# Performance work log

Measured on AMD Instinct MI355X. Metric: run time of the kernel, lower is better.

## Reference

```python
import jax, jax.numpy as jnp
import numpy as np

D_MODEL = 1024
N_HEADS = 16
N_KV_HEADS = 4
HEAD_DIM = 64   # d_model // total_n_heads
KEY_DIM = 64    # defaults to head_dim
N_REP = N_HEADS // N_KV_HEADS
ATTN_SCALE = 1.0 / np.sqrt(HEAD_DIM)
B, S = 2, 2048


def apply_rope(x, cos, sin):
    # x: [B,S,H,Dh]; cos/sin: [S,Dh//2]; pairs are (x[2j], x[2j+1]) per llama-style apply_rotary_emb
    xr, xi = x[..., ::2], x[..., 1::2]
    c = cos[None, :, None, :]
    s = sin[None, :, None, :]
    out_r = xr * c - xi * s
    out_i = xr * s + xi * c
    return jnp.stack([out_r, out_i], axis=-1).reshape(x.shape)


def setup_inputs() -> dict:
    key = jax.random.key(0)
    ks = jax.random.split(key, 7)
    query = jax.random.normal(ks[0], (B, S, D_MODEL), jnp.float32)
    k_in = jax.random.normal(ks[1], (B, S, D_MODEL), jnp.float32)
    v_in = jax.random.normal(ks[2], (B, S, D_MODEL), jnp.float32)
    # real RoPE frequency tables (theta=10000)
    inv_freq = 1.0 / (10000.0 ** (np.arange(0, KEY_DIM, 2, dtype=np.float32) / KEY_DIM))
    ang = np.outer(np.arange(S, dtype=np.float32), inv_freq)  # [S, KEY_DIM//2]
    freqs_cos = jnp.asarray(np.cos(ang), jnp.float32)
    freqs_sin = jnp.asarray(np.sin(ang), jnp.float32)
    sc = D_MODEL ** -0.5
    wq = jax.random.normal(ks[3], (N_HEADS * KEY_DIM, D_MODEL), jnp.float32) * sc
    wk = jax.random.normal(ks[4], (N_KV_HEADS * KEY_DIM, D_MODEL), jnp.float32) * sc
    wv = jax.random.normal(ks[5], (N_KV_HEADS * HEAD_DIM, D_MODEL), jnp.float32) * sc
    wo = jax.random.normal(ks[6], (N_HEADS * HEAD_DIM, N_HEADS * HEAD_DIM), jnp.float32) * sc
    return {"query": query, "key": k_in, "value": v_in,
            "freqs_cos": freqs_cos, "freqs_sin": freqs_sin,
            "wq": wq, "wk": wk, "wv": wv, "wo": wo}


def reference(query, key, value, freqs_cos, freqs_sin, wq, wk, wv, wo):
    b, sq, _ = query.shape
    sk = key.shape[1]
    xq = (query @ wq.T).reshape(b, sq, N_HEADS, KEY_DIM)
    xk = (key @ wk.T).reshape(b, sk, N_KV_HEADS, KEY_DIM)
    xv = (value @ wv.T).reshape(b, sk, N_KV_HEADS, HEAD_DIM)
    xq = apply_rope(xq, freqs_cos, freqs_sin)
    xk = apply_rope(xk, freqs_cos, freqs_sin)
    # GQA: repeat kv heads (equivalent to torch repeat_kv expand+reshape)
    xk = jnp.repeat(xk, N_REP, axis=2)
    xv = jnp.repeat(xv, N_REP, axis=2)
    scores = jnp.einsum('bqhd,bkhd->bhqk', xq, xk) * ATTN_SCALE
    causal = jnp.tril(jnp.ones((sq, sk), dtype=bool))
    scores = jnp.where(causal[None, None, :, :], scores, -jnp.inf)
    attn = jax.nn.softmax(scores, axis=-1)
    out = jnp.einsum('bhqk,bkhd->bqhd', attn, xv).reshape(b, sq, N_HEADS * HEAD_DIM)
    return out @ wo.T
```

## Files before the change

### kernel.cpp

```cpp
#include <hip/hip_runtime.h>

#define DM 1024
#define NHEADS 16
#define NKVH 4
#define HDIM 64
#define NB 2
#define SEQ 2048
#define MTOK (NB*SEQ)

typedef __attribute__((ext_vector_type(4))) float f32x4;
typedef __attribute__((ext_vector_type(8))) short short8;
typedef unsigned short u16;
typedef unsigned int u32;

__device__ __forceinline__ u16 f2b(float f) {
  u32 i; __builtin_memcpy(&i, &f, 4);
  u32 r = i + 0x7fffu + ((i >> 16) & 1u);
  return (u16)(r >> 16);
}
__device__ __forceinline__ u32 cvtpk(float a, float b) {
  u32 r; asm("v_cvt_pk_bf16_f32 %0, %1, %2" : "=v"(r) : "v"(a), "v"(b)); return r;
}
__device__ __forceinline__ void gload16(const void* g, void* l) {
  __builtin_amdgcn_global_load_lds((const __attribute__((address_space(1))) u32*)g,
                                   (__attribute__((address_space(3))) u32*)l, 16, 0, 0);
}

__global__ __launch_bounds__(256) void gemm_qkv(const float* __restrict__ Aq, const float* __restrict__ Ak,
                                                const float* __restrict__ Av, const float* __restrict__ wq,
                                                const float* __restrict__ wk, const float* __restrict__ wv,
                                                const float* __restrict__ cosb, const float* __restrict__ sinb,
                                                u16* __restrict__ Qr, u16* __restrict__ Kr,
                                                u16* __restrict__ Vt) {
  __shared__ __attribute__((aligned(16))) u16 SH[13824];
  u16* As = SH;
  u16* Bs = SH + 4608;
  const int tid = threadIdx.x, lane = tid & 63, w = tid >> 6;
  const int wr = w >> 1, wc = w & 1, lo = lane & 15, hi = lane >> 4;
  const int bx = blockIdx.x, by = blockIdx.y;
  const int m0 = bx * 64;

  const float *Ap, *Wp;
  int n0, mode;
  if (by < 8) { Ap = Aq; Wp = wq; n0 = by * 128; mode = 0; }
  else if (by < 10) { Ap = Ak; Wp = wk; n0 = (by - 8) * 128; mode = 1; }
  else { Ap = Av; Wp = wv; n0 = (by - 10) * 128; mode = 2; }

  const int srw = tid >> 2, sc0 = (tid & 3) * 4;
  const float* Abase = Ap + (size_t)(m0 + srw) * DM + sc0;
  const float* Wbase = Wp + (size_t)(n0 + srw) * DM + sc0;

  f32x4 acc[2][4];
#pragma unroll
  for (int i = 0; i < 2; i++)
#pragma unroll
    for (int j = 0; j < 4; j++) acc[i][j] = (f32x4){0.f, 0.f, 0.f, 0.f};

  float4 ra[4], rb[8];
#pragma unroll
  for (int j = 0; j < 4; j++) ra[j] = *(const float4*)(Abase + j * 16);
#pragma unroll
  for (int s = 0; s < 2; s++)
#pragma unroll
    for (int j = 0; j < 4; j++) rb[s * 4 + j] = *(const float4*)(Wbase + (size_t)s * 64 * DM + j * 16);

  for (int ks = 0; ks < 16; ks++) {
#pragma unroll
    for (int j = 0; j < 4; j++) {
      u32 w2[2] = {cvtpk(ra[j].x, ra[j].y), cvtpk(ra[j].z, ra[j].w)};
      *(uint2*)&As[srw * 72 + sc0 + j * 16] = *(uint2*)w2;
    }
#pragma unroll
    for (int s = 0; s < 2; s++)
#pragma unroll
      for (int j = 0; j < 4; j++) {
        u32 w2[2] = {cvtpk(rb[s * 4 + j].x, rb[s * 4 + j].y), cvtpk(rb[s * 4 + j].z, rb[s * 4 + j].w)};
        *(uint2*)&Bs[(s * 64 + srw) * 72 + sc0 + j * 16] = *(uint2*)w2;
      }
    __syncthreads();
    if (ks < 15) {
      const int k1 = (ks + 1) * 64;
#pragma unroll
      for (int j = 0; j < 4; j++) ra[j] = *(const float4*)(Abase + k1 + j * 16);
#pragma unroll
      for (int s = 0; s < 2; s++)
#pragma unroll
        for (int j = 0; j < 4; j++)
          rb[s * 4 + j] = *(const float4*)(Wbase + (size_t)s * 64 * DM + k1 + j * 16);
    }
    short8 af[2][2], bfr[4][2];
#pragma unroll
    for (int mi = 0; mi < 2; mi++)
#pragma unroll
      for (int kk = 0; kk < 2; kk++)
        af[mi][kk] = *(const short8*)(&As[(wr * 32 + mi * 16 + lo) * 72 + kk * 32 + hi * 8]);
#pragma unroll
    for (int ni = 0; ni < 4; ni++)
#pragma unroll
      for (int kk = 0; kk < 2; kk++)
        bfr[ni][kk] = *(const short8*)(&Bs[(wc * 64 + ni * 16 + lo) * 72 + kk * 32 + hi * 8]);
    __builtin_amdgcn_s_setprio(1);
#pragma unroll
    for (int mi = 0; mi < 2; mi++)
#pragma unroll
      for (int ni = 0; ni < 4; ni++) {
        acc[mi][ni] = __builtin_amdgcn_mfma_f32_16x16x32_bf16(af[mi][0], bfr[ni][0], acc[mi][ni], 0, 0, 0);
        acc[mi][ni] = __builtin_amdgcn_mfma_f32_16x16x32_bf16(af[mi][1], bfr[ni][1], acc[mi][ni], 0, 0, 0);
      }
    __builtin_amdgcn_s_setprio(0);
    __syncthreads();
  }

  if (mode < 2) {
    const float scale = (mode == 0) ? 0.18033688f : 1.0f;
    u16* outp = (mode == 0) ? Qr : Kr;
    const int OH = (mode == 0) ? NHEADS : NKVH;
    const float sgn = (lo & 1) ? 1.0f : -1.0f;
#pragma unroll
    for (int ni = 0; ni < 4; ni++) {
      const int col = n0 + wc * 64 + ni * 16 + lo;
      const int h = col >> 6, d = col & 63, j = d >> 1;
#pragma unroll
      for (int mi = 0; mi < 2; mi++)
#pragma unroll
        for (int r = 0; r < 4; r++) {
          int row = m0 + wr * 32 + mi * 16 + hi * 4 + r;
          int srow = row & (SEQ - 1), bb = row >> 11;
          float v = acc[mi][ni][r];
          float pv = __shfl_xor(v, 1, 64);
          float c = cosb[srow * 32 + j];
          float s = sinb[srow * 32 + j];
          outp[((size_t)(bb * OH + h) * SEQ + srow) * 64 + d] = f2b((v * c + pv * s * sgn) * scale);
        }
    }
  } else {
    u16* Tt = SH;
#pragma unroll
    for (int mi = 0; mi < 2; mi++)
#pragma unroll
      for (int ni = 0; ni < 4; ni++) {
        const int cl = wc * 64 + ni * 16 + lo;
#pragma unroll
        for (int r = 0; r < 4; r++) {
          int rl = wr * 32 + mi * 16 + hi * 4 + r;
          Tt[cl * 72 + rl] = f2b(acc[mi][ni][r]);
        }
      }
    __syncthreads();
    const int dl = tid >> 1;
    const int sh2 = (tid & 1) * 32;
    const int dg = n0 + dl;
    const int kh = dg >> 6, drow = dg & 63;
    const int bb = m0 >> 11, sbase = m0 & (SEQ - 1);
    u16* dst = Vt + ((size_t)(bb * NKVH + kh) * 64 + drow) * SEQ + sbase + sh2;
#pragma unroll
    for (int i = 0; i < 4; i++)
      *(uint4*)(dst + i * 8) = *(const uint4*)&Tt[dl * 72 + sh2 + i * 8];
  }
}

__device__ __forceinline__ void softmax_pv(f32x4 (&sc)[4], float& m, float& lsp, f32x4 (&o)[4],
                                           const short8* vb0, const short8* vb1, int hi) {
  float lm = sc[0][0];
#pragma unroll
  for (int f = 0; f < 4; f++)
#pragma unroll
    for (int r = 0; r < 4; r++) lm = fmaxf(lm, sc[f][r]);
  if (__any(lm - m > 8.f)) {
    float mx = fmaxf(m, lm);
    mx = fmaxf(mx, __shfl_xor(mx, 16, 64));
    mx = fmaxf(mx, __shfl_xor(mx, 32, 64));
    float corr = exp2f(m - mx);
    m = mx;
    lsp *= corr;
    float corrq[4];
#pragma unroll
    for (int r = 0; r < 4; r++) corrq[r] = __shfl(corr, hi * 4 + r, 64);
#pragma unroll
    for (int nf = 0; nf < 4; nf++)
#pragma unroll
      for (int r = 0; r < 4; r++) o[nf][r] *= corrq[r];
  }
  float pv2[4][4];
#pragma unroll
  for (int f = 0; f < 4; f++)
#pragma unroll
    for (int r = 0; r < 4; r++) {
      pv2[f][r] = exp2f(sc[f][r] - m);
      lsp += pv2[f][r];
    }
  union { u32 u[4]; short8 s8; } pa0, pa1;
#pragma unroll
  for (int t = 0; t < 4; t++) {
    int fsel = t >> 1, r0 = 2 * (t & 1);
    pa0.u[t] = cvtpk(pv2[fsel][r0], pv2[fsel][r0 + 1]);
    pa1.u[t] = cvtpk(pv2[2 + fsel][r0], pv2[2 + fsel][r0 + 1]);
  }
  __builtin_amdgcn_s_setprio(1);
#pragma unroll
  for (int nf = 0; nf < 4; nf++) {
    o[nf] = __builtin_amdgcn_mfma_f32_16x16x32_bf16(pa0.s8, vb0[nf], o[nf], 0, 0, 0);
    o[nf] = __builtin_amdgcn_mfma_f32_16x16x32_bf16(pa1.s8, vb1[nf], o[nf], 0, 0, 0);
  }
  __builtin_amdgcn_s_setprio(0);
}

__global__ __launch_bounds__(256, 2) void attn_kernel(const u16* __restrict__ Q, const u16* __restrict__ Kb,
                                                      const u16* __restrict__ Vt, u16* __restrict__ AO) {
  __shared__ __attribute__((aligned(16))) u16 Ks[2][4096];
  __shared__ __attribute__((aligned(16))) u16 Vs[2][4096];
  const int tid = threadIdx.x;
  const int w = tid >> 6, lane = tid & 63;
  const int lo = lane & 15, hi = lane >> 4;
  const int bh = blockIdx.x;
  const int b = bh >> 4, h = bh & 15, kh = h >> 2;
  const int p = blockIdx.y;
  const int tA = p, tB = 31 - p;
  const int q0A = tA * 64 + w * 16;
  const int q0B = tB * 64 + w * 16;
  const u16* Qp = Q + (size_t)bh * SEQ * 64;
  const u16* Kp = Kb + (size_t)(b * NKVH + kh) * SEQ * 64;
  const u16* Vp = Vt + (size_t)(b * NKVH + kh) * 64 * SEQ;

  short8 qfA[2], qfB[2];
#pragma unroll
  for (int kk = 0; kk < 2; kk++) {
    qfA[kk] = *(const short8*)(Qp + (size_t)(q0A + lo) * 64 + kk * 32 + hi * 8);
    qfB[kk] = *(const short8*)(Qp + (size_t)(q0B + lo) * 64 + kk * 32 + hi * 8);
  }

  f32x4 oA[4], oB[4];
#pragma unroll
  for (int nf = 0; nf < 4; nf++) { oA[nf] = (f32x4){0.f,0.f,0.f,0.f}; oB[nf] = (f32x4){0.f,0.f,0.f,0.f}; }
  float mA = -__builtin_inff(), lspA = 0.f;
  float mB = -__builtin_inff(), lspB = 0.f;

  auto key = [](int row) { return (row & 3) | (((row >> 3) & 1) << 2); };
  auto stage = [&](int kv0, int bufi) {
#pragma unroll
    for (int s = 0; s < 2; s++) {
      int base = s * 4096 + w * 1024;
      int o2 = base + (lane << 4);
      int row = o2 >> 7;
      int gg = ((o2 >> 4) & 7) ^ key(row);
      gload16(Kp + (size_t)(kv0 + row) * 64 + gg * 8, (char*)&Ks[bufi][0] + base);
      gload16(Vp + (size_t)row * SEQ + kv0 + gg * 8, (char*)&Vs[bufi][0] + base);
    }
  };
  auto lds8 = [&](const u16* S, int row, int col8) {
    return *(const short8*)(S + row * 64 + (col8 ^ (key(row) << 3)));
  };

  int krow[4];
#pragma unroll
  for (int f = 0; f < 4; f++)
    krow[f] = 32 * (f >> 1) + 8 * (lo >> 2) + 4 * (f & 1) + (lo & 3);

  const int nt = tB + 1;
  stage(0, 0);
  __syncthreads();

  for (int c = 0; c < nt; ++c) {
    const int cur = c & 1;
    const int kv0 = c * 64;
    if (c + 1 < nt) stage(kv0 + 64, cur ^ 1);

    short8 kf0[4], kf1[4];
#pragma unroll
    for (int f = 0; f < 4; f++) {
      kf0[f] = lds8(&Ks[cur][0], krow[f], hi * 8);
      kf1[f] = lds8(&Ks[cur][0], krow[f], 32 + hi * 8);
    }
    const bool actA = (c <= tA);

    f32x4 scB[4], scA[4];
#pragma unroll
    for (int f = 0; f < 4; f++) scB[f] = (f32x4){0.f,0.f,0.f,0.f};
    __builtin_amdgcn_s_setprio(1);
#pragma unroll
    for (int f = 0; f < 4; f++) {
      scB[f] = __builtin_amdgcn_mfma_f32_16x16x32_bf16(kf0[f], qfB[0], scB[f], 0, 0, 0);
      scB[f] = __builtin_amdgcn_mfma_f32_16x16x32_bf16(kf1[f], qfB[1], scB[f], 0, 0, 0);
    }
    __builtin_amdgcn_s_setprio(0);
    if (actA) {
#pragma unroll
      for (int f = 0; f < 4; f++) scA[f] = (f32x4){0.f,0.f,0.f,0.f};
      __builtin_amdgcn_s_setprio(1);
#pragma unroll
      for (int f = 0; f < 4; f++) {
        scA[f] = __builtin_amdgcn_mfma_f32_16x16x32_bf16(kf0[f], qfA[0], scA[f], 0, 0, 0);
        scA[f] = __builtin_amdgcn_mfma_f32_16x16x32_bf16(kf1[f], qfA[1], scA[f], 0, 0, 0);
      }
      __builtin_amdgcn_s_setprio(0);
    }

    short8 vb0[4], vb1[4];
#pragma unroll
    for (int nf = 0; nf < 4; nf++) {
      vb0[nf] = lds8(&Vs[cur][0], nf * 16 + lo, hi * 8);
      vb1[nf] = lds8(&Vs[cur][0], nf * 16 + lo, 32 + hi * 8);
    }

    if (c == tB) {
#pragma unroll
      for (int f = 0; f < 4; f++) {
        int kvb = kv0 + 32 * (f >> 1) + 8 * hi + 4 * (f & 1);
#pragma unroll
        for (int r = 0; r < 4; r++)
          if (kvb + r > q0B + lo) scB[f][r] = -__builtin_inff();
      }
    }
    softmax_pv(scB, mB, lspB, oB, vb0, vb1, hi);

    if (actA) {
      if (c == tA) {
#pragma unroll
        for (int f = 0; f < 4; f++) {
          int kvb = kv0 + 32 * (f >> 1) + 8 * hi + 4 * (f & 1);
#pragma unroll
          for (int r = 0; r < 4; r++)
            if (kvb + r > q0A + lo) scA[f][r] = -__builtin_inff();
        }
      }
      softmax_pv(scA, mA, lspA, oA, vb0, vb1, hi);
    }
    __syncthreads();
  }

#pragma unroll
  for (int t2 = 0; t2 < 2; t2++) {
    float lsp = t2 ? lspB : lspA;
    const int q0 = t2 ? q0B : q0A;
    f32x4* o = t2 ? oB : oA;
    lsp += __shfl_xor(lsp, 16, 64);
    lsp += __shfl_xor(lsp, 32, 64);
    float inv = 1.0f / lsp;
    float invq[4];
#pragma unroll
    for (int r = 0; r < 4; r++) invq[r] = __shfl(inv, hi * 4 + r, 64);
#pragma unroll
    for (int nf = 0; nf < 4; nf++)
#pragma unroll
      for (int r = 0; r < 4; r++) {
        int q = q0 + hi * 4 + r;
        int d = nf * 16 + lo;
        AO[((size_t)(b * SEQ + q) * NHEADS + h) * 64 + d] = f2b(o[nf][r] * invq[r]);
      }
  }
}

__global__ __launch_bounds__(256) void gemm_out(const u16* __restrict__ A, const float* __restrict__ W,
                                                float* __restrict__ Out) {
  __shared__ __attribute__((aligned(16))) u16 As[4096];
  __shared__ __attribute__((aligned(16))) u16 Bs[9216];
  const int tid = threadIdx.x, lane = tid & 63, w = tid >> 6;
  const int wr = w >> 1, wc = w & 1, lo = lane & 15, hi = lane >> 4;
  const int m0 = blockIdx.x * 64, n0 = blockIdx.y * 128;
  const int crow = lane >> 3;
  const int gsw = ((lane & 7) ^ crow) << 3;

  f32x4 acc[2][4];
#pragma unroll
  for (int i = 0; i < 2; i++)
#pragma unroll
    for (int j = 0; j < 4; j++) acc[i][j] = (f32x4){0.f, 0.f, 0.f, 0.f};

  const int srw = tid >> 2, sc0 = (tid & 3) * 4;
  const float* Wbase = W + (size_t)(n0 + srw) * DM + sc0;
  float4 rb[8];
#pragma unroll
  for (int s = 0; s < 2; s++)
#pragma unroll
    for (int j = 0; j < 4; j++) rb[s * 4 + j] = *(const float4*)(Wbase + (size_t)s * 64 * DM + j * 16);

  for (int ks = 0; ks < 16; ks++) {
    const int k0 = ks * 64;
#pragma unroll
    for (int cc = 0; cc < 2; ++cc) {
      int c = w * 2 + cc;
      gload16(A + (size_t)(m0 + c * 8 + crow) * DM + k0 + gsw, &As[c * 512]);
    }
#pragma unroll
    for (int s = 0; s < 2; s++)
#pragma unroll
      for (int j = 0; j < 4; j++) {
        u32 w2[2] = {cvtpk(rb[s * 4 + j].x, rb[s * 4 + j].y), cvtpk(rb[s * 4 + j].z, rb[s * 4 + j].w)};
        *(uint2*)&Bs[(s * 64 + srw) * 72 + sc0 + j * 16] = *(uint2*)w2;
      }
    __syncthreads();
    if (ks < 15) {
      const int k1 = k0 + 64;
#pragma unroll
      for (int s = 0; s < 2; s++)
#pragma unroll
        for (int j = 0; j < 4; j++)
          rb[s * 4 + j] = *(const float4*)(Wbase + (size_t)s * 64 * DM + k1 + j * 16);
    }
    short8 af[2][2], bfr[4][2];
#pragma unroll
    for (int mi = 0; mi < 2; mi++)
#pragma unroll
      for (int kk = 0; kk < 2; kk++)
        af[mi][kk] = *(const short8*)(&As[(wr * 32 + mi * 16 + lo) * 64 + (((kk * 4 + hi) ^ (lo & 7)) << 3)]);
#pragma unroll
    for (int ni = 0; ni < 4; ni++)
#pragma unroll
      for (int kk = 0; kk < 2; kk++)
        bfr[ni][kk] = *(const short8*)(&Bs[(wc * 64 + ni * 16 + lo) * 72 + kk * 32 + hi * 8]);
    __builtin_amdgcn_s_setprio(1);
#pragma unroll
    for (int mi = 0; mi < 2; mi++)
#pragma unroll
      for (int ni = 0; ni < 4; ni++) {
        acc[mi][ni] = __builtin_amdgcn_mfma_f32_16x16x32_bf16(af[mi][0], bfr[ni][0], acc[mi][ni], 0, 0, 0);
        acc[mi][ni] = __builtin_amdgcn_mfma_f32_16x16x32_bf16(af[mi][1], bfr[ni][1], acc[mi][ni], 0, 0, 0);
      }
    __builtin_amdgcn_s_setprio(0);
    __syncthreads();
  }

#pragma unroll
  for (int mi = 0; mi < 2; mi++)
#pragma unroll
    for (int ni = 0; ni < 4; ni++)
#pragma unroll
      for (int r = 0; r < 4; r++) {
        int row = m0 + wr * 32 + mi * 16 + hi * 4 + r;
        int col = n0 + wc * 64 + ni * 16 + lo;
        Out[(size_t)row * DM + col] = acc[mi][ni][r];
      }
}

extern "C" void kernel_launch(void* const* d_in, const int* in_sizes, int n_in,
                              void* d_out, int out_size, void* d_ws, size_t ws_size,
                              hipStream_t stream) {
  const float* query = (const float*)d_in[0];
  const float* key_ = (const float*)d_in[1];
  const float* value = (const float*)d_in[2];
  const float* fcos = (const float*)d_in[3];
  const float* fsin = (const float*)d_in[4];
  const float* wq = (const float*)d_in[5];
  const float* wk = (const float*)d_in[6];
  const float* wv = (const float*)d_in[7];
  const float* wo = (const float*)d_in[8];

  char* ws = (char*)d_ws;
  size_t off = 0;
  auto alloc = [&](size_t elems) {
    u16* p = (u16*)(ws + off);
    off = (off + elems * 2 + 255) & ~(size_t)255;
    return p;
  };
  u16* Qr = alloc((size_t)MTOK * DM);
  u16* Kr = alloc((size_t)NB * NKVH * SEQ * 64);
  u16* Vt = alloc((size_t)NB * NKVH * 64 * SEQ);
  u16* AO = alloc((size_t)MTOK * DM);

  gemm_qkv<<<dim3(64, 12), 256, 0, stream>>>(query, key_, value, wq, wk, wv,
                                             fcos, fsin, Qr, Kr, Vt);

  attn_kernel<<<dim3(NB * NHEADS, 16), 256, 0, stream>>>(Qr, Kr, Vt, AO);

  gemm_out<<<dim3(64, 8), 256, 0, stream>>>(AO, wo, (float*)d_out);
}
```

Before: 98.88 us.

## Pre-convert inputs and weights to bf16 and stage GEMM tiles via direct LDS loads

Adds a conversion kernel that turns the fp32 activations and all weights into bf16 buffers before the GEMMs. Both GEMMs then load tiles straight into swizzled LDS with global_load_lds instead of loading fp32 into registers and converting per tile, and their occupancy hints are raised. This removes per-tile conversion and register staging, at the cost of an extra kernel launch and a full extra read and write of the inputs. The attention kernel's blockIdx.y to tile-pair mapping is also reordered.

```diff
diff --git a/kernel.cpp b/kernel.cpp
--- a/kernel.cpp
+++ b/kernel.cpp
@@ -26,29 +26,76 @@
                                    (__attribute__((address_space(3))) u32*)l, 16, 0, 0);
 }
 
-__global__ __launch_bounds__(256) void gemm_qkv(const float* __restrict__ Aq, const float* __restrict__ Ak,
-                                                const float* __restrict__ Av, const float* __restrict__ wq,
-                                                const float* __restrict__ wk, const float* __restrict__ wv,
-                                                const float* __restrict__ cosb, const float* __restrict__ sinb,
-                                                u16* __restrict__ Qr, u16* __restrict__ Kr,
-                                                u16* __restrict__ Vt) {
-  __shared__ __attribute__((aligned(16))) u16 SH[13824];
+__device__ __forceinline__ void cvt8(const float* __restrict__ src, u16* __restrict__ dst, int i) {
+  float4 a = *(const float4*)(src + i);
+  float4 b = *(const float4*)(src + i + 4);
+  uint4 pk;
+  pk.x = cvtpk(a.x, a.y);
+  pk.y = cvtpk(a.z, a.w);
+  pk.z = cvtpk(b.x, b.y);
+  pk.w = cvtpk(b.z, b.w);
+  *(uint4*)(dst + i) = pk;
+}
+
+__global__ __launch_bounds__(256) void cvt_all(const float* __restrict__ q, const float* __restrict__ k,
+                                               const float* __restrict__ v, const float* __restrict__ wq,
+                                               const float* __restrict__ wk, const float* __restrict__ wv,
+                                               const float* __restrict__ wo, u16* oq, u16* ok, u16* ov,
+                                               u16* owq, u16* owk, u16* owv, u16* owo) {
+  const int ACT = (MTOK * DM) / 2048;
+  const int BIG = (DM * DM) / 2048;
+  const int SML = (256 * DM) / 2048;
+  int bid = blockIdx.x;
+  const float* s; u16* d;
+  if (bid < ACT) { s = q; d = oq; }
+  else if (bid < 2 * ACT) { s = k; d = ok; bid -= ACT; }
+  else if (bid < 3 * ACT) { s = v; d = ov; bid -= 2 * ACT; }
+  else {
+    bid -= 3 * ACT;
+    if (bid < BIG) { s = wq; d = owq; }
+    else if (bid < 2 * BIG) { s = wo; d = owo; bid -= BIG; }
+    else if (bid < 2 * BIG + SML) { s = wk; d = owk; bid -= 2 * BIG; }
+    else { s = wv; d = owv; bid -= 2 * BIG + SML; }
+  }
+  cvt8(s, d, (bid * 256 + threadIdx.x) * 8);
+}
+
+template<int NR>
+__device__ __forceinline__ void stage_tile(const u16* __restrict__ src, int k0, u16* lds,
+                                           int w, int lane) {
+#pragma unroll
+  for (int i = 0; i < NR / 32; i++) {
+    const int base = (i * 4 + w) * 1024;
+    const int row = (base >> 7) + (lane >> 3);
+    const int g = lane & 7;
+    gload16(src + (size_t)row * DM + k0 + ((g ^ (row & 7)) << 3), (char*)lds + base);
+  }
+}
+__device__ __forceinline__ short8 lds_frag(const u16* L, int row, int gr) {
+  return *(const short8*)(L + row * 64 + ((gr ^ (row & 7)) << 3));
+}
+
+__global__ __launch_bounds__(256, 3) void gemm_qkv(const u16* __restrict__ Aq, const u16* __restrict__ Ak,
+                                                   const u16* __restrict__ Av, const u16* __restrict__ wq,
+                                                   const u16* __restrict__ wk, const u16* __restrict__ wv,
+                                                   const float* __restrict__ cosb, const float* __restrict__ sinb,
+                                                   u16* __restrict__ Qr, u16* __restrict__ Kr,
+                                                   u16* __restrict__ Vt) {
+  __shared__ __attribute__((aligned(16))) u16 SH[12288];
   u16* As = SH;
-  u16* Bs = SH + 4608;
+  u16* Bs = SH + 4096;
   const int tid = threadIdx.x, lane = tid & 63, w = tid >> 6;
   const int wr = w >> 1, wc = w & 1, lo = lane & 15, hi = lane >> 4;
   const int bx = blockIdx.x, by = blockIdx.y;
   const int m0 = bx * 64;
 
-  const float *Ap, *Wp;
+  const u16 *Ap, *Wp;
   int n0, mode;
   if (by < 8) { Ap = Aq; Wp = wq; n0 = by * 128; mode = 0; }
   else if (by < 10) { Ap = Ak; Wp = wk; n0 = (by - 8) * 128; mode = 1; }
   else { Ap = Av; Wp = wv; n0 = (by - 10) * 128; mode = 2; }
-
-  const int srw = tid >> 2, sc0 = (tid & 3) * 4;
-  const float* Abase = Ap + (size_t)(m0 + srw) * DM + sc0;
-  const float* Wbase = Wp + (size_t)(n0 + srw) * DM + sc0;
+  const u16* Abase = Ap + (size_t)m0 * DM;
+  const u16* Wbase = Wp + (size_t)n0 * DM;
 
   f32x4 acc[2][4];
 #pragma unroll
@@ -56,49 +103,22 @@
 #pragma unroll
     for (int j = 0; j < 4; j++) acc[i][j] = (f32x4){0.f, 0.f, 0.f, 0.f};
 
-  float4 ra[4], rb[8];
-#pragma unroll
-  for (int j = 0; j < 4; j++) ra[j] = *(const float4*)(Abase + j * 16);
-#pragma unroll
-  for (int s = 0; s < 2; s++)
-#pragma unroll
-    for (int j = 0; j < 4; j++) rb[s * 4 + j] = *(const float4*)(Wbase + (size_t)s * 64 * DM + j * 16);
-
   for (int ks = 0; ks < 16; ks++) {
-#pragma unroll
-    for (int j = 0; j < 4; j++) {
-      u32 w2[2] = {cvtpk(ra[j].x, ra[j].y), cvtpk(ra[j].z, ra[j].w)};
-      *(uint2*)&As[srw * 72 + sc0 + j * 16] = *(uint2*)w2;
-    }
-#pragma unroll
-    for (int s = 0; s < 2; s++)
-#pragma unroll
-      for (int j = 0; j < 4; j++) {
-        u32 w2[2] = {cvtpk(rb[s * 4 + j].x, rb[s * 4 + j].y), cvtpk(rb[s * 4 + j].z, rb[s * 4 + j].w)};
-        *(uint2*)&Bs[(s * 64 + srw) * 72 + sc0 + j * 16] = *(uint2*)w2;
-      }
-    __syncthreads();
-    if (ks < 15) {
-      const int k1 = (ks + 1) * 64;
-#pragma unroll
-      for (int j = 0; j < 4; j++) ra[j] = *(const float4*)(Abase + k1 + j * 16);
-#pragma unroll
-      for (int s = 0; s < 2; s++)
-#pragma unroll
-        for (int j = 0; j < 4; j++)
-          rb[s * 4 + j] = *(const float4*)(Wbase + (size_t)s * 64 * DM + k1 + j * 16);
-    }
+    const int k0 = ks * 64;
+    stage_tile<64>(Abase, k0, As, w, lane);
+    stage_tile<128>(Wbase, k0, Bs, w, lane);
+    __syncthreads();
     short8 af[2][2], bfr[4][2];
 #pragma unroll
     for (int mi = 0; mi < 2; mi++)
 #pragma unroll
       for (int kk = 0; kk < 2; kk++)
-        af[mi][kk] = *(const short8*)(&As[(wr * 32 + mi * 16 + lo) * 72 + kk * 32 + hi * 8]);
+        af[mi][kk] = lds_frag(As, wr * 32 + mi * 16 + lo, kk * 4 + hi);
 #pragma unroll
     for (int ni = 0; ni < 4; ni++)
 #pragma unroll
       for (int kk = 0; kk < 2; kk++)
-        bfr[ni][kk] = *(const short8*)(&Bs[(wc * 64 + ni * 16 + lo) * 72 + kk * 32 + hi * 8]);
+        bfr[ni][kk] = lds_frag(Bs, wc * 64 + ni * 16 + lo, kk * 4 + hi);
     __builtin_amdgcn_s_setprio(1);
 #pragma unroll
     for (int mi = 0; mi < 2; mi++)
@@ -214,7 +234,8 @@
   const int lo = lane & 15, hi = lane >> 4;
   const int bh = blockIdx.x;
   const int b = bh >> 4, h = bh & 15, kh = h >> 2;
-  const int p = blockIdx.y;
+  const int yy = blockIdx.y;
+  const int p = (yy < 8) ? yy : 23 - yy;
   const int tA = p, tB = 31 - p;
   const int q0A = tA * 64 + w * 16;
   const int q0B = tB * 64 + w * 16;
@@ -350,64 +371,39 @@
   }
 }
 
-__global__ __launch_bounds__(256) void gemm_out(const u16* __restrict__ A, const float* __restrict__ W,
-                                                float* __restrict__ Out) {
-  __shared__ __attribute__((aligned(16))) u16 As[4096];
-  __shared__ __attribute__((aligned(16))) u16 Bs[9216];
+__global__ __launch_bounds__(256, 2) void gemm_out(const u16* __restrict__ A, const u16* __restrict__ W,
+                                                   float* __restrict__ Out) {
+  __shared__ __attribute__((aligned(16))) u16 SH[12288];
+  u16* As = SH;
+  u16* Bs = SH + 4096;
   const int tid = threadIdx.x, lane = tid & 63, w = tid >> 6;
   const int wr = w >> 1, wc = w & 1, lo = lane & 15, hi = lane >> 4;
   const int m0 = blockIdx.x * 64, n0 = blockIdx.y * 128;
-  const int crow = lane >> 3;
-  const int gsw = ((lane & 7) ^ crow) << 3;
+  const u16* Abase = A + (size_t)m0 * DM;
+  const u16* Wbase = W + (size_t)n0 * DM;
 
   f32x4 acc[2][4];
 #pragma unroll
   for (int i = 0; i < 2; i++)
 #pragma unroll
     for (int j = 0; j < 4; j++) acc[i][j] = (f32x4){0.f, 0.f, 0.f, 0.f};
-
-  const int srw = tid >> 2, sc0 = (tid & 3) * 4;
-  const float* Wbase = W + (size_t)(n0 + srw) * DM + sc0;
-  float4 rb[8];
-#pragma unroll
-  for (int s = 0; s < 2; s++)
-#pragma unroll
-    for (int j = 0; j < 4; j++) rb[s * 4 + j] = *(const float4*)(Wbase + (size_t)s * 64 * DM + j * 16);
 
   for (int ks = 0; ks < 16; ks++) {
     const int k0 = ks * 64;
-#pragma unroll
-    for (int cc = 0; cc < 2; ++cc) {
-      int c = w * 2 + cc;
-      gload16(A + (size_t)(m0 + c * 8 + crow) * DM + k0 + gsw, &As[c * 512]);
-    }
-#pragma unroll
-    for (int s = 0; s < 2; s++)
-#pragma unroll
-      for (int j = 0; j < 4; j++) {
-        u32 w2[2] = {cvtpk(rb[s * 4 + j].x, rb[s * 4 + j].y), cvtpk(rb[s * 4 + j].z, rb[s * 4 + j].w)};
-        *(uint2*)&Bs[(s * 64 + srw) * 72 + sc0 + j * 16] = *(uint2*)w2;
-      }
-    __syncthreads();
-    if (ks < 15) {
-      const int k1 = k0 + 64;
-#pragma unroll
-      for (int s = 0; s < 2; s++)
-#pragma unroll
-        for (int j = 0; j < 4; j++)
-          rb[s * 4 + j] = *(const float4*)(Wbase + (size_t)s * 64 * DM + k1 + j * 16);
-    }
+    stage_tile<64>(Abase, k0, As, w, lane);
+    stage_tile<128>(Wbase, k0, Bs, w, lane);
+    __syncthreads();
     short8 af[2][2], bfr[4][2];
 #pragma unroll
     for (int mi = 0; mi < 2; mi++)
 #pragma unroll
       for (int kk = 0; kk < 2; kk++)
-        af[mi][kk] = *(const short8*)(&As[(wr * 32 + mi * 16 + lo) * 64 + (((kk * 4 + hi) ^ (lo & 7)) << 3)]);
+        af[mi][kk] = lds_frag(As, wr * 32 + mi * 16 + lo, kk * 4 + hi);
 #pragma unroll
     for (int ni = 0; ni < 4; ni++)
 #pragma unroll
       for (int kk = 0; kk < 2; kk++)
-        bfr[ni][kk] = *(const short8*)(&Bs[(wc * 64 + ni * 16 + lo) * 72 + kk * 32 + hi * 8]);
+        bfr[ni][kk] = lds_frag(Bs, wc * 64 + ni * 16 + lo, kk * 4 + hi);
     __builtin_amdgcn_s_setprio(1);
 #pragma unroll
     for (int mi = 0; mi < 2; mi++)
@@ -452,15 +448,25 @@
     off = (off + elems * 2 + 255) & ~(size_t)255;
     return p;
   };
+  u16* qf = alloc((size_t)MTOK * DM);
+  u16* kf = alloc((size_t)MTOK * DM);
+  u16* vf = alloc((size_t)MTOK * DM);
+  u16* wqf = alloc((size_t)DM * DM);
+  u16* wkf = alloc((size_t)256 * DM);
+  u16* wvf = alloc((size_t)256 * DM);
+  u16* wof = alloc((size_t)DM * DM);
   u16* Qr = alloc((size_t)MTOK * DM);
   u16* Kr = alloc((size_t)NB * NKVH * SEQ * 64);
   u16* Vt = alloc((size_t)NB * NKVH * 64 * SEQ);
   u16* AO = alloc((size_t)MTOK * DM);
 
-  gemm_qkv<<<dim3(64, 12), 256, 0, stream>>>(query, key_, value, wq, wk, wv,
+  cvt_all<<<3 * 2048 + 1280, 256, 0, stream>>>(query, key_, value, wq, wk, wv, wo,
+                                               qf, kf, vf, wqf, wkf, wvf, wof);
+
+  gemm_qkv<<<dim3(64, 12), 256, 0, stream>>>(qf, kf, vf, wqf, wkf, wvf,
                                              fcos, fsin, Qr, Kr, Vt);
 
   attn_kernel<<<dim3(NB * NHEADS, 16), 256, 0, stream>>>(Qr, Kr, Vt, AO);
 
-  gemm_out<<<dim3(64, 8), 256, 0, stream>>>(AO, wo, (float*)d_out);
-}
+  gemm_out<<<dim3(64, 8), 256, 0, stream>>>(AO, wof, (float*)d_out);
+}
```

Result: faster. 93.50 us (-5.4%).
